# Kernel optimization log

Measured on AMD Instinct MI355X. Metric: run time of the kernel, lower is better.

## Reference

```python
import jax, jax.numpy as jnp
import numpy as np

N_NODES = 50000
N_EDGES = 800000
IN_CH = 128
OUT_CH = 64  # hidden = 2*OUT_CH = 128


def setup_inputs() -> dict:
    key = jax.random.key(0)
    ks = jax.random.split(key, 5)
    x = jax.random.normal(ks[0], (N_NODES, IN_CH), dtype=jnp.float32)
    edge_index = jax.random.randint(ks[1], (2, N_EDGES), 0, N_NODES, dtype=jnp.int32)
    # Glorot-ish scaled weights for the two GCNConv layers
    W1 = jax.random.normal(ks[2], (IN_CH, 2 * OUT_CH), dtype=jnp.float32) * 0.05
    b1 = jnp.zeros((2 * OUT_CH,), dtype=jnp.float32)
    W2 = jax.random.normal(ks[3], (2 * OUT_CH, OUT_CH), dtype=jnp.float32) * 0.05
    b2 = jnp.zeros((OUT_CH,), dtype=jnp.float32)
    return {"x": x, "edge_index": edge_index, "W1": W1, "b1": b1, "W2": W2, "b2": b2}


def reference(x, edge_index, W1, b1, W2, b2):
    N = x.shape[0]
    # GCN normalization with self-loops (PyG GCNConv default):
    # A_hat = A + I, deg from target nodes, norm = d_i^-1/2 * d_j^-1/2
    loops = jnp.arange(N, dtype=edge_index.dtype)
    row = jnp.concatenate([edge_index[0], loops])  # source
    col = jnp.concatenate([edge_index[1], loops])  # target
    deg = jax.ops.segment_sum(jnp.ones(row.shape, x.dtype), col, num_segments=N)
    dinv = jnp.where(deg > 0, jax.lax.rsqrt(deg), 0.0)
    norm = dinv[row] * dinv[col]  # [E+N]

    def conv(h, W, b):
        h = h @ W                           # [N, D_out] transform first (D_out <= D_in path)
        msg = norm[:, None] * h[row]        # gather + scale: [E+N, D_out]
        agg = jax.ops.segment_sum(msg, col, num_segments=N)
        return agg + b

    h = jax.nn.relu(conv(x, W1, b1))
    return conv(h, W2, b2)
```

## Files before the change

### kernel.cpp

```cpp
#include <hip/hip_runtime.h>
#include <hip/hip_bf16.h>
#include <hip/hip_fp16.h>

#define IN_CH  128
#define HID    128
#define OUTC   64

#define SCAN_CHUNK 2048
#define NBLK1 128
#define CHUNK2 6400
#define CAP2  6144

typedef _Float16 half8 __attribute__((ext_vector_type(8)));
typedef _Float16 half4v __attribute__((ext_vector_type(4)));
typedef float float4v __attribute__((ext_vector_type(4)));

__global__ __launch_bounds__(256) void histA_kernel(const int* __restrict__ dst,
                                                    int* __restrict__ hist,
                                                    int E, int NBK, int chunk) {
    __shared__ int h[256];
    int t = threadIdx.x;
    h[t] = 0;
    __syncthreads();
    int base = blockIdx.x * chunk;
    int end = base + chunk; if (end > E) end = E;
    for (int e = base + t; e < end; e += 256)
        atomicAdd(&h[dst[e] >> 8], 1);
    __syncthreads();
    if (t < NBK) hist[t * NBLK1 + blockIdx.x] = h[t];
}

__global__ __launch_bounds__(256) void gscanA_kernel(const int* __restrict__ arr,
                                                     int* __restrict__ bsum, int n) {
    __shared__ int red[256];
    int t = threadIdx.x;
    int base = blockIdx.x * SCAN_CHUNK + t * 8;
    int s = 0;
#pragma unroll
    for (int k = 0; k < 8; ++k) { int i = base + k; if (i < n) s += arr[i]; }
    red[t] = s;
    __syncthreads();
    for (int d = 128; d > 0; d >>= 1) {
        if (t < d) red[t] += red[t + d];
        __syncthreads();
    }
    if (t == 0) bsum[blockIdx.x] = red[0];
}

__global__ void gscanB_kernel(const int* __restrict__ bsum, int* __restrict__ boff, int nb) {
    if (threadIdx.x == 0 && blockIdx.x == 0) {
        int run = 0;
        for (int b = 0; b < nb; ++b) { boff[b] = run; run += bsum[b]; }
    }
}

__global__ __launch_bounds__(256) void gscanC_kernel(int* __restrict__ arr,
                                                     const int* __restrict__ boff, int n) {
    __shared__ int sums[256];
    int t = threadIdx.x;
    int base = blockIdx.x * SCAN_CHUNK + t * 8;
    int c[8];
    int s = 0;
#pragma unroll
    for (int k = 0; k < 8; ++k) { int i = base + k; c[k] = (i < n) ? arr[i] : 0; s += c[k]; }
    sums[t] = s;
    __syncthreads();
    for (int d = 1; d < 256; d <<= 1) {
        int v = (t >= d) ? sums[t - d] : 0;
        __syncthreads();
        sums[t] += v;
        __syncthreads();
    }
    int run = boff[blockIdx.x] + ((t == 0) ? 0 : sums[t - 1]);
#pragma unroll
    for (int k = 0; k < 8; ++k) {
        int i = base + k;
        if (i < n) { arr[i] = run; run += c[k]; }
    }
}

__global__ __launch_bounds__(256) void scatter2_kernel(const int* __restrict__ src,
                                                       const int* __restrict__ dst,
                                                       const int* __restrict__ HS,
                                                       unsigned* __restrict__ tmp,
                                                       int E, int NBK, int chunk) {
    __shared__ unsigned ein[CHUNK2];
    __shared__ unsigned eout[CHUNK2];
    __shared__ int h[256], lex[256], cur[256], hs[256];
    int t = threadIdx.x, blk = blockIdx.x;
    int base = blk * chunk;
    int end = base + chunk; if (end > E) end = E;
    int n = end - base;

    h[t] = 0;
    if (t < NBK) hs[t] = HS[t * NBLK1 + blk];
    __syncthreads();
    for (int i = t; i < n; i += 256) {
        unsigned d = (unsigned)dst[base + i];
        unsigned s = (unsigned)src[base + i];
        unsigned v = (d << 16) | s;
        ein[i] = v;
        atomicAdd(&h[d >> 8], 1);
    }
    __syncthreads();
    int c = h[t];
    for (int d = 1; d < 256; d <<= 1) {
        int v = (t >= d) ? h[t - d] : 0;
        __syncthreads();
        h[t] += v;
        __syncthreads();
    }
    lex[t] = h[t] - c;
    cur[t] = h[t] - c;
    __syncthreads();
    for (int i = t; i < n; i += 256) {
        unsigned v = ein[i];
        int pos = atomicAdd(&cur[v >> 24], 1);
        eout[pos] = v;
    }
    __syncthreads();
    for (int i = t; i < n; i += 256) {
        unsigned v = eout[i];
        int b = v >> 24;
        tmp[hs[b] + i - lex[b]] = v;
    }
}

__global__ __launch_bounds__(256) void csr2_kernel(const unsigned* __restrict__ tmp,
                                                   const int* __restrict__ HS,
                                                   int* __restrict__ off,
                                                   ushort* __restrict__ srcs,
                                                   float* __restrict__ dinv,
                                                   int E, int N, int NBK) {
    __shared__ int h[256];
    __shared__ int cur[256];
    __shared__ ushort outb[CAP2];
    int b = blockIdx.x, t = threadIdx.x;
    int lo = HS[b * NBLK1];
    int hi = (b + 1 < NBK) ? HS[(b + 1) * NBLK1] : E;

    h[t] = 0;
    __syncthreads();
    for (int i = lo + t; i < hi; i += 256)
        atomicAdd(&h[(tmp[i] >> 16) & 255], 1);
    __syncthreads();
    int c = h[t];
    for (int d = 1; d < 256; d <<= 1) {
        int v = (t >= d) ? h[t - d] : 0;
        __syncthreads();
        h[t] += v;
        __syncthreads();
    }
    int excl = h[t] - c;
    int node = (b << 8) + t;
    if (node < N) {
        off[node] = lo + excl;
        dinv[node] = rsqrtf((float)(c + 1));
    }
    if (b == NBK - 1 && t == 0) off[N] = E;
    cur[t] = excl;
    __syncthreads();
    for (int i = lo + t; i < hi; i += 256) {
        unsigned v = tmp[i];
        int pos = atomicAdd(&cur[(v >> 16) & 255], 1);
        if (pos < CAP2) outb[pos] = (ushort)(v & 0xFFFFu);
        else srcs[lo + pos] = (ushort)(v & 0xFFFFu);
    }
    __syncthreads();
    int cnt_b = hi - lo; if (cnt_b > CAP2) cnt_b = CAP2;
    for (int i = t; i < cnt_b; i += 256) srcs[lo + i] = outb[i];
}

__global__ void prep_kernel(const float* __restrict__ x,
                            const float* __restrict__ dinv,
                            _Float16* __restrict__ xhs,
                            const float* __restrict__ W1, const float* __restrict__ W2,
                            _Float16* __restrict__ Wt1, _Float16* __restrict__ Wt2,
                            int n4) {
    int i = blockIdx.x * 256 + threadIdx.x;
    if (i < n4) {
        float d = dinv[i >> 5];
        float4 v = ((const float4*)x)[i];
        half4v o = { (_Float16)(d * v.x), (_Float16)(d * v.y),
                     (_Float16)(d * v.z), (_Float16)(d * v.w) };
        ((half4v*)xhs)[i] = o;
    } else {
        int j = i - n4;
        if (j < 128 * 128) {
            int k = j >> 7, nn = j & 127;
            Wt1[nn * 128 + k] = (_Float16)W1[j];
        } else if (j < 128 * 128 + 128 * 64) {
            int jj = j - 128 * 128;
            int k = jj >> 6, nn = jj & 63;
            Wt2[nn * 128 + k] = (_Float16)W2[jj];
        }
    }
}

template <int NC, bool BIASRELU, bool SCALE>
__global__ __launch_bounds__(256) void mfma_gemm_kernel(const _Float16* A,
                                                        const _Float16* __restrict__ Wt,
                                                        const float* __restrict__ bias,
                                                        const float* __restrict__ dinv,
                                                        _Float16* Y, int N) {
    int wave = threadIdx.x >> 6;
    int lane = threadIdx.x & 63;
    int n16 = lane & 15;
    int q   = lane >> 4;
    int rowBase = blockIdx.x * 128 + wave * 32;

    half8 a[2][4];
#pragma unroll
    for (int rt = 0; rt < 2; ++rt) {
        int row = rowBase + rt * 16 + n16;
        if (row >= N) row = N - 1;
        const _Float16* ap = A + (size_t)row * 128 + q * 8;
#pragma unroll
        for (int kb = 0; kb < 4; ++kb)
            a[rt][kb] = *(const half8*)(ap + kb * 32);
    }

    constexpr int NT = NC / 16;
    float4v acc[2][NT];
#pragma unroll
    for (int rt = 0; rt < 2; ++rt)
#pragma unroll
        for (int ct = 0; ct < NT; ++ct) acc[rt][ct] = (float4v)0.f;

#pragma unroll
    for (int ct = 0; ct < NT; ++ct) {
        const _Float16* bp = Wt + (size_t)(ct * 16 + n16) * 128 + q * 8;
        half8 b[4];
#pragma unroll
        for (int kb = 0; kb < 4; ++kb) b[kb] = *(const half8*)(bp + kb * 32);
#pragma unroll
        for (int kb = 0; kb < 4; ++kb) {
            acc[0][ct] = __builtin_amdgcn_mfma_f32_16x16x32_f16(a[0][kb], b[kb], acc[0][ct], 0, 0, 0);
            acc[1][ct] = __builtin_amdgcn_mfma_f32_16x16x32_f16(a[1][kb], b[kb], acc[1][ct], 0, 0, 0);
        }
    }

#pragma unroll
    for (int rt = 0; rt < 2; ++rt) {
#pragma unroll
        for (int ct = 0; ct < NT; ++ct) {
            int col = ct * 16 + n16;
            float bv = BIASRELU ? bias[col] : 0.f;
#pragma unroll
            for (int r = 0; r < 4; ++r) {
                int row = rowBase + rt * 16 + q * 4 + r;
                if (row < N) {
                    float v = acc[rt][ct][r];
                    if (BIASRELU) v = fmaxf(v + bv, 0.f);
                    if (SCALE) v *= dinv[row];
                    Y[(size_t)row * NC + col] = (_Float16)v;
                }
            }
        }
    }
}

__global__ __launch_bounds__(256) void agg1_kernel(const _Float16* __restrict__ xhs,
                                                   const float* __restrict__ x,
                                                   const int* __restrict__ off,
                                                   const ushort* __restrict__ srcs,
                                                   const float* __restrict__ dinv,
                                                   _Float16* __restrict__ A1, int N) {
    int node = blockIdx.x * 4 + (threadIdx.x >> 6);
    if (node >= N) return;
    int lane = threadIdx.x & 63;
    int p = lane & 15;
    int g = lane >> 4;
    int s = off[node], e = off[node + 1];

    float acc[8];
#pragma unroll
    for (int i = 0; i < 8; ++i) acc[i] = 0.f;

    const half8* xs = (const half8*)xhs;
    int j = s;
    for (; j + 16 <= e; j += 16) {
        int i0 = srcs[j + g];
        int i1 = srcs[j + 4 + g];
        int i2 = srcs[j + 8 + g];
        int i3 = srcs[j + 12 + g];
        half8 u0 = xs[(size_t)i0 * 16 + p];
        half8 u1 = xs[(size_t)i1 * 16 + p];
        half8 u2 = xs[(size_t)i2 * 16 + p];
        half8 u3 = xs[(size_t)i3 * 16 + p];
#pragma unroll
        for (int i = 0; i < 8; ++i)
            acc[i] += ((float)u0[i] + (float)u1[i]) + ((float)u2[i] + (float)u3[i]);
    }
    for (; j < e; j += 4) {
        int jj = j + g;
        if (jj < e) {
            int i0 = srcs[jj];
            half8 u0 = xs[(size_t)i0 * 16 + p];
#pragma unroll
            for (int i = 0; i < 8; ++i) acc[i] += (float)u0[i];
        }
    }
#pragma unroll
    for (int i = 0; i < 8; ++i) {
        acc[i] += __shfl_xor(acc[i], 16, 64);
        acc[i] += __shfl_xor(acc[i], 32, 64);
    }
    if (g == 0) {
        float di = dinv[node];
        const float4* xr = (const float4*)(x + (size_t)node * 128);
        float4 s0 = xr[2 * p], s1 = xr[2 * p + 1];
        half8 h;
        h[0] = (_Float16)(di * (acc[0] + di * s0.x));
        h[1] = (_Float16)(di * (acc[1] + di * s0.y));
        h[2] = (_Float16)(di * (acc[2] + di * s0.z));
        h[3] = (_Float16)(di * (acc[3] + di * s0.w));
        h[4] = (_Float16)(di * (acc[4] + di * s1.x));
        h[5] = (_Float16)(di * (acc[5] + di * s1.y));
        h[6] = (_Float16)(di * (acc[6] + di * s1.z));
        h[7] = (_Float16)(di * (acc[7] + di * s1.w));
        *((half8*)(A1 + (size_t)node * 128) + p) = h;
    }
}

__global__ __launch_bounds__(256) void agg2_kernel(const _Float16* __restrict__ H3s,
                                                   const int* __restrict__ off,
                                                   const ushort* __restrict__ srcs,
                                                   const float* __restrict__ dinv,
                                                   const float* __restrict__ bias,
                                                   float* __restrict__ out, int N) {
    int node = blockIdx.x * 4 + (threadIdx.x >> 6);
    if (node >= N) return;
    int lane = threadIdx.x & 63;
    int p = lane & 7;
    int g = lane >> 3;
    int s = off[node], e = off[node + 1];

    float acc[8];
#pragma unroll
    for (int i = 0; i < 8; ++i) acc[i] = 0.f;

    const half8* hs = (const half8*)H3s;
    int j = s;
    for (; j + 16 <= e; j += 16) {
        int i0 = srcs[j + g];
        int i1 = srcs[j + 8 + g];
        half8 u0 = hs[(size_t)i0 * 8 + p];
        half8 u1 = hs[(size_t)i1 * 8 + p];
#pragma unroll
        for (int i = 0; i < 8; ++i) acc[i] += (float)u0[i] + (float)u1[i];
    }
    for (; j < e; j += 8) {
        int jj = j + g;
        if (jj < e) {
            int i0 = srcs[jj];
            half8 u0 = hs[(size_t)i0 * 8 + p];
#pragma unroll
            for (int i = 0; i < 8; ++i) acc[i] += (float)u0[i];
        }
    }
#pragma unroll
    for (int i = 0; i < 8; ++i) {
        acc[i] += __shfl_xor(acc[i], 8, 64);
        acc[i] += __shfl_xor(acc[i], 16, 64);
        acc[i] += __shfl_xor(acc[i], 32, 64);
    }
    if (g == 0) {
        float di = dinv[node];
        half8 sv = hs[(size_t)node * 8 + p];
        const float4* bp = (const float4*)(bias + p * 8);
        float4 b0 = bp[0], b1 = bp[1];
        float4 o0, o1;
        o0.x = di * (acc[0] + (float)sv[0]) + b0.x;
        o0.y = di * (acc[1] + (float)sv[1]) + b0.y;
        o0.z = di * (acc[2] + (float)sv[2]) + b0.z;
        o0.w = di * (acc[3] + (float)sv[3]) + b0.w;
        o1.x = di * (acc[4] + (float)sv[4]) + b1.x;
        o1.y = di * (acc[5] + (float)sv[5]) + b1.y;
        o1.z = di * (acc[6] + (float)sv[6]) + b1.z;
        o1.w = di * (acc[7] + (float)sv[7]) + b1.w;
        float4* op = (float4*)(out + (size_t)node * 64 + p * 8);
        op[0] = o0; op[1] = o1;
    }
}

extern "C" void kernel_launch(void* const* d_in, const int* in_sizes, int n_in,
                              void* d_out, int out_size, void* d_ws, size_t ws_size,
                              hipStream_t stream) {
    const float* x   = (const float*)d_in[0];
    const int*   ei  = (const int*)d_in[1];
    const float* W1  = (const float*)d_in[2];
    const float* b1  = (const float*)d_in[3];
    const float* W2  = (const float*)d_in[4];
    const float* b2  = (const float*)d_in[5];
    float* out = (float*)d_out;

    const int N = in_sizes[0] / IN_CH;
    const int E = in_sizes[1] / 2;
    const int* src = ei;
    const int* dst = ei + E;

    const int NBK = (N + 255) >> 8;
    const int M   = NBK * NBLK1;
    const int NB2 = (M + SCAN_CHUNK - 1) / SCAN_CHUNK;
    const int chunk = (E + NBLK1 - 1) / NBLK1;

    auto align256 = [](size_t v) { return (v + 255) & ~(size_t)255; };
    char* w = (char*)d_ws;
    int* off = (int*)w;              w += align256((size_t)(N + 1) * 4);
    ushort* srcs = (ushort*)w;       w += align256((size_t)E * 2);
    float* dinv = (float*)w;         w += align256((size_t)N * 4);
    int* hist = (int*)w;             w += align256((size_t)M * 4);
    int* bs2 = (int*)w;              w += align256((size_t)NB2 * 4);
    int* bo2 = (int*)w;              w += align256((size_t)NB2 * 4);
    _Float16* Wt1 = (_Float16*)w;    w += align256((size_t)HID * 128 * 2);
    _Float16* Wt2 = (_Float16*)w;    w += align256((size_t)OUTC * 128 * 2);
    _Float16* A1 = (_Float16*)w;
    unsigned* tmp = (unsigned*)w;
    w += align256((size_t)N * HID * 2);
    _Float16* xhs = (_Float16*)w;
    _Float16* H3s = (_Float16*)w;
    w += align256((size_t)N * HID * 2);

    histA_kernel<<<NBLK1, 256, 0, stream>>>(dst, hist, E, NBK, chunk);
    gscanA_kernel<<<NB2, 256, 0, stream>>>(hist, bs2, M);
    gscanB_kernel<<<1, 64, 0, stream>>>(bs2, bo2, NB2);
    gscanC_kernel<<<NB2, 256, 0, stream>>>(hist, bo2, M);
    scatter2_kernel<<<NBLK1, 256, 0, stream>>>(src, dst, hist, tmp, E, NBK, chunk);
    csr2_kernel<<<NBK, 256, 0, stream>>>(tmp, hist, off, srcs, dinv, E, N, NBK);

    int n4 = N * IN_CH / 4;
    int prep_grid = (n4 + 128 * 128 + 128 * 64 + 255) / 256;
    prep_kernel<<<prep_grid, 256, 0, stream>>>(x, dinv, xhs, W1, W2, Wt1, Wt2, n4);

    agg1_kernel<<<(N + 3) / 4, 256, 0, stream>>>(xhs, x, off, srcs, dinv, A1, N);
    mfma_gemm_kernel<HID, true, false><<<(N + 127) / 128, 256, 0, stream>>>(A1, Wt1, b1, nullptr, A1, N);

    mfma_gemm_kernel<OUTC, false, true><<<(N + 127) / 128, 256, 0, stream>>>(A1, Wt2, nullptr, dinv, H3s, N);
    agg2_kernel<<<(N + 3) / 4, 256, 0, stream>>>(H3s, off, srcs, dinv, b2, out, N);
}
```

Baseline: 212.7 us.

## Fuse CSR build into cooperative megakernel and fuse two GEMMs via LDS

Replaces the seven preprocessing launches (histogram, three-stage scan, scatter, CSR build, prep) with one cooperative kernel that uses grid.sync between phases. This removes launch gaps and tiny serial kernels. The two MFMA GEMMs are also fused: the ReLU'd hidden tile is staged in shared memory and multiplied by W2 directly, which avoids writing and re-reading A1. The costs are grid-wide barriers on only 256 blocks, a large static LDS footprint in the megakernel, and a strided elementwise prep loop.

```diff
diff --git a/kernel.cpp b/kernel.cpp
--- a/kernel.cpp
+++ b/kernel.cpp
@@ -1,101 +1,83 @@
 #include <hip/hip_runtime.h>
 #include <hip/hip_bf16.h>
 #include <hip/hip_fp16.h>
+#include <hip/hip_cooperative_groups.h>
+
+namespace cg = cooperative_groups;
 
 #define IN_CH  128
 #define HID    128
 #define OUTC   64
 
-#define SCAN_CHUNK 2048
-#define NBLK1 128
-#define CHUNK2 6400
-#define CAP2  6144
+#define GRIDC  256
+#define EMAX_CHUNK 3200
+#define CAP2   6144
 
 typedef _Float16 half8 __attribute__((ext_vector_type(8)));
 typedef _Float16 half4v __attribute__((ext_vector_type(4)));
 typedef float float4v __attribute__((ext_vector_type(4)));
 
-__global__ __launch_bounds__(256) void histA_kernel(const int* __restrict__ dst,
-                                                    int* __restrict__ hist,
-                                                    int E, int NBK, int chunk) {
-    __shared__ int h[256];
-    int t = threadIdx.x;
+__global__ __launch_bounds__(256) void mega_kernel(
+        const int* __restrict__ src, const int* __restrict__ dst,
+        int* __restrict__ hist, int* __restrict__ bsum, int* __restrict__ boff,
+        int* __restrict__ off, ushort* __restrict__ srcs, float* __restrict__ dinv,
+        unsigned* __restrict__ tmp,
+        const float* __restrict__ x, _Float16* __restrict__ xhs,
+        const float* __restrict__ W1, const float* __restrict__ W2,
+        _Float16* __restrict__ Wt1, _Float16* __restrict__ Wt2,
+        int E, int N, int NBK) {
+    cg::grid_group grid = cg::this_grid();
+    __shared__ int h[256], cur[256], lex[256], hs[256];
+    __shared__ unsigned ein[EMAX_CHUNK], eout[EMAX_CHUNK];
+    __shared__ ushort outb[CAP2];
+
+    int t = threadIdx.x, blk = blockIdx.x;
+    const int chunkE = (E + GRIDC - 1) / GRIDC;
+    int base = blk * chunkE;
+    int end = base + chunkE; if (end > E) end = E;
+
     h[t] = 0;
     __syncthreads();
-    int base = blockIdx.x * chunk;
-    int end = base + chunk; if (end > E) end = E;
     for (int e = base + t; e < end; e += 256)
         atomicAdd(&h[dst[e] >> 8], 1);
     __syncthreads();
-    if (t < NBK) hist[t * NBLK1 + blockIdx.x] = h[t];
-}
-
-__global__ __launch_bounds__(256) void gscanA_kernel(const int* __restrict__ arr,
-                                                     int* __restrict__ bsum, int n) {
-    __shared__ int red[256];
-    int t = threadIdx.x;
-    int base = blockIdx.x * SCAN_CHUNK + t * 8;
-    int s = 0;
-#pragma unroll
-    for (int k = 0; k < 8; ++k) { int i = base + k; if (i < n) s += arr[i]; }
-    red[t] = s;
-    __syncthreads();
-    for (int d = 128; d > 0; d >>= 1) {
-        if (t < d) red[t] += red[t + d];
-        __syncthreads();
-    }
-    if (t == 0) bsum[blockIdx.x] = red[0];
-}
-
-__global__ void gscanB_kernel(const int* __restrict__ bsum, int* __restrict__ boff, int nb) {
-    if (threadIdx.x == 0 && blockIdx.x == 0) {
-        int run = 0;
-        for (int b = 0; b < nb; ++b) { boff[b] = run; run += bsum[b]; }
-    }
-}
-
-__global__ __launch_bounds__(256) void gscanC_kernel(int* __restrict__ arr,
-                                                     const int* __restrict__ boff, int n) {
-    __shared__ int sums[256];
-    int t = threadIdx.x;
-    int base = blockIdx.x * SCAN_CHUNK + t * 8;
-    int c[8];
-    int s = 0;
-#pragma unroll
-    for (int k = 0; k < 8; ++k) { int i = base + k; c[k] = (i < n) ? arr[i] : 0; s += c[k]; }
-    sums[t] = s;
+    if (t < NBK) hist[t * GRIDC + blk] = h[t];
+    grid.sync();
+
+    int v2 = (t < NBK) ? hist[blk * NBK + t] : 0;
+    h[t] = v2;
     __syncthreads();
     for (int d = 1; d < 256; d <<= 1) {
-        int v = (t >= d) ? sums[t - d] : 0;
-        __syncthreads();
-        sums[t] += v;
-        __syncthreads();
-    }
-    int run = boff[blockIdx.x] + ((t == 0) ? 0 : sums[t - 1]);
-#pragma unroll
-    for (int k = 0; k < 8; ++k) {
-        int i = base + k;
-        if (i < n) { arr[i] = run; run += c[k]; }
-    }
-}
-
-__global__ __launch_bounds__(256) void scatter2_kernel(const int* __restrict__ src,
-                                                       const int* __restrict__ dst,
-                                                       const int* __restrict__ HS,
-                                                       unsigned* __restrict__ tmp,
-                                                       int E, int NBK, int chunk) {
-    __shared__ unsigned ein[CHUNK2];
-    __shared__ unsigned eout[CHUNK2];
-    __shared__ int h[256], lex[256], cur[256], hs[256];
-    int t = threadIdx.x, blk = blockIdx.x;
-    int base = blk * chunk;
-    int end = base + chunk; if (end > E) end = E;
-    int n = end - base;
+        int u = (t >= d) ? h[t - d] : 0;
+        __syncthreads();
+        h[t] += u;
+        __syncthreads();
+    }
+    if (t == 255) bsum[blk] = h[255];
+    grid.sync();
+
+    if (blk == 0) {
+        int bv = bsum[t];
+        cur[t] = bv;
+        __syncthreads();
+        for (int d = 1; d < 256; d <<= 1) {
+            int u = (t >= d) ? cur[t - d] : 0;
+            __syncthreads();
+            cur[t] += u;
+            __syncthreads();
+        }
+        boff[t] = cur[t] - bv;
+    }
+    grid.sync();
+
+    if (t < NBK) hist[blk * NBK + t] = boff[blk] + (h[t] - v2);
+    grid.sync();
 
     h[t] = 0;
-    if (t < NBK) hs[t] = HS[t * NBLK1 + blk];
-    __syncthreads();
-    for (int i = t; i < n; i += 256) {
+    if (t < NBK) hs[t] = hist[t * GRIDC + blk];
+    __syncthreads();
+    int n3 = end - base;
+    for (int i = t; i < n3; i += 256) {
         unsigned d = (unsigned)dst[base + i];
         unsigned s = (unsigned)src[base + i];
         unsigned v = (d << 16) | s;
@@ -103,158 +85,83 @@
         atomicAdd(&h[d >> 8], 1);
     }
     __syncthreads();
-    int c = h[t];
+    int c3 = h[t];
     for (int d = 1; d < 256; d <<= 1) {
-        int v = (t >= d) ? h[t - d] : 0;
-        __syncthreads();
-        h[t] += v;
-        __syncthreads();
-    }
-    lex[t] = h[t] - c;
-    cur[t] = h[t] - c;
-    __syncthreads();
-    for (int i = t; i < n; i += 256) {
+        int u = (t >= d) ? h[t - d] : 0;
+        __syncthreads();
+        h[t] += u;
+        __syncthreads();
+    }
+    lex[t] = h[t] - c3;
+    cur[t] = h[t] - c3;
+    __syncthreads();
+    for (int i = t; i < n3; i += 256) {
         unsigned v = ein[i];
         int pos = atomicAdd(&cur[v >> 24], 1);
         eout[pos] = v;
     }
     __syncthreads();
-    for (int i = t; i < n; i += 256) {
+    for (int i = t; i < n3; i += 256) {
         unsigned v = eout[i];
         int b = v >> 24;
         tmp[hs[b] + i - lex[b]] = v;
     }
-}
-
-__global__ __launch_bounds__(256) void csr2_kernel(const unsigned* __restrict__ tmp,
-                                                   const int* __restrict__ HS,
-                                                   int* __restrict__ off,
-                                                   ushort* __restrict__ srcs,
-                                                   float* __restrict__ dinv,
-                                                   int E, int N, int NBK) {
-    __shared__ int h[256];
-    __shared__ int cur[256];
-    __shared__ ushort outb[CAP2];
-    int b = blockIdx.x, t = threadIdx.x;
-    int lo = HS[b * NBLK1];
-    int hi = (b + 1 < NBK) ? HS[(b + 1) * NBLK1] : E;
-
-    h[t] = 0;
-    __syncthreads();
-    for (int i = lo + t; i < hi; i += 256)
-        atomicAdd(&h[(tmp[i] >> 16) & 255], 1);
-    __syncthreads();
-    int c = h[t];
-    for (int d = 1; d < 256; d <<= 1) {
-        int v = (t >= d) ? h[t - d] : 0;
-        __syncthreads();
-        h[t] += v;
-        __syncthreads();
-    }
-    int excl = h[t] - c;
-    int node = (b << 8) + t;
-    if (node < N) {
-        off[node] = lo + excl;
-        dinv[node] = rsqrtf((float)(c + 1));
-    }
-    if (b == NBK - 1 && t == 0) off[N] = E;
-    cur[t] = excl;
-    __syncthreads();
-    for (int i = lo + t; i < hi; i += 256) {
-        unsigned v = tmp[i];
-        int pos = atomicAdd(&cur[(v >> 16) & 255], 1);
-        if (pos < CAP2) outb[pos] = (ushort)(v & 0xFFFFu);
-        else srcs[lo + pos] = (ushort)(v & 0xFFFFu);
-    }
-    __syncthreads();
-    int cnt_b = hi - lo; if (cnt_b > CAP2) cnt_b = CAP2;
-    for (int i = t; i < cnt_b; i += 256) srcs[lo + i] = outb[i];
-}
-
-__global__ void prep_kernel(const float* __restrict__ x,
-                            const float* __restrict__ dinv,
-                            _Float16* __restrict__ xhs,
-                            const float* __restrict__ W1, const float* __restrict__ W2,
-                            _Float16* __restrict__ Wt1, _Float16* __restrict__ Wt2,
-                            int n4) {
-    int i = blockIdx.x * 256 + threadIdx.x;
-    if (i < n4) {
-        float d = dinv[i >> 5];
-        float4 v = ((const float4*)x)[i];
-        half4v o = { (_Float16)(d * v.x), (_Float16)(d * v.y),
-                     (_Float16)(d * v.z), (_Float16)(d * v.w) };
-        ((half4v*)xhs)[i] = o;
-    } else {
-        int j = i - n4;
-        if (j < 128 * 128) {
-            int k = j >> 7, nn = j & 127;
-            Wt1[nn * 128 + k] = (_Float16)W1[j];
-        } else if (j < 128 * 128 + 128 * 64) {
-            int jj = j - 128 * 128;
-            int k = jj >> 6, nn = jj & 63;
-            Wt2[nn * 128 + k] = (_Float16)W2[jj];
-        }
-    }
-}
-
-template <int NC, bool BIASRELU, bool SCALE>
-__global__ __launch_bounds__(256) void mfma_gemm_kernel(const _Float16* A,
-                                                        const _Float16* __restrict__ Wt,
-                                                        const float* __restrict__ bias,
-                                                        const float* __restrict__ dinv,
-                                                        _Float16* Y, int N) {
-    int wave = threadIdx.x >> 6;
-    int lane = threadIdx.x & 63;
-    int n16 = lane & 15;
-    int q   = lane >> 4;
-    int rowBase = blockIdx.x * 128 + wave * 32;
-
-    half8 a[2][4];
-#pragma unroll
-    for (int rt = 0; rt < 2; ++rt) {
-        int row = rowBase + rt * 16 + n16;
-        if (row >= N) row = N - 1;
-        const _Float16* ap = A + (size_t)row * 128 + q * 8;
-#pragma unroll
-        for (int kb = 0; kb < 4; ++kb)
-            a[rt][kb] = *(const half8*)(ap + kb * 32);
-    }
-
-    constexpr int NT = NC / 16;
-    float4v acc[2][NT];
-#pragma unroll
-    for (int rt = 0; rt < 2; ++rt)
-#pragma unroll
-        for (int ct = 0; ct < NT; ++ct) acc[rt][ct] = (float4v)0.f;
-
-#pragma unroll
-    for (int ct = 0; ct < NT; ++ct) {
-        const _Float16* bp = Wt + (size_t)(ct * 16 + n16) * 128 + q * 8;
-        half8 b[4];
-#pragma unroll
-        for (int kb = 0; kb < 4; ++kb) b[kb] = *(const half8*)(bp + kb * 32);
-#pragma unroll
-        for (int kb = 0; kb < 4; ++kb) {
-            acc[0][ct] = __builtin_amdgcn_mfma_f32_16x16x32_f16(a[0][kb], b[kb], acc[0][ct], 0, 0, 0);
-            acc[1][ct] = __builtin_amdgcn_mfma_f32_16x16x32_f16(a[1][kb], b[kb], acc[1][ct], 0, 0, 0);
-        }
-    }
-
-#pragma unroll
-    for (int rt = 0; rt < 2; ++rt) {
-#pragma unroll
-        for (int ct = 0; ct < NT; ++ct) {
-            int col = ct * 16 + n16;
-            float bv = BIASRELU ? bias[col] : 0.f;
-#pragma unroll
-            for (int r = 0; r < 4; ++r) {
-                int row = rowBase + rt * 16 + q * 4 + r;
-                if (row < N) {
-                    float v = acc[rt][ct][r];
-                    if (BIASRELU) v = fmaxf(v + bv, 0.f);
-                    if (SCALE) v *= dinv[row];
-                    Y[(size_t)row * NC + col] = (_Float16)v;
-                }
+    grid.sync();
+
+    if (blk < NBK) {
+        int lo = hist[blk * GRIDC];
+        int hi = (blk + 1 < NBK) ? hist[(blk + 1) * GRIDC] : E;
+        h[t] = 0;
+        __syncthreads();
+        for (int i = lo + t; i < hi; i += 256)
+            atomicAdd(&h[(tmp[i] >> 16) & 255], 1);
+        __syncthreads();
+        int c = h[t];
+        for (int d = 1; d < 256; d <<= 1) {
+            int u = (t >= d) ? h[t - d] : 0;
+            __syncthreads();
+            h[t] += u;
+            __syncthreads();
+        }
+        int excl = h[t] - c;
+        int node = (blk << 8) + t;
+        if (node < N) {
+            off[node] = lo + excl;
+            dinv[node] = rsqrtf((float)(c + 1));
+        }
+        if (blk == NBK - 1 && t == 0) off[N] = E;
+        cur[t] = excl;
+        __syncthreads();
+        for (int i = lo + t; i < hi; i += 256) {
+            unsigned v = tmp[i];
+            int pos = atomicAdd(&cur[(v >> 16) & 255], 1);
+            if (pos < CAP2) outb[pos] = (ushort)(v & 0xFFFFu);
+            else srcs[lo + pos] = (ushort)(v & 0xFFFFu);
+        }
+        __syncthreads();
+        int cnt_b = hi - lo; if (cnt_b > CAP2) cnt_b = CAP2;
+        for (int i = t; i < cnt_b; i += 256) srcs[lo + i] = outb[i];
+    }
+    grid.sync();
+
+    int n4 = N * (IN_CH / 4);
+    int total = n4 + 128 * 128 + 128 * 64;
+    for (int i = blk * 256 + t; i < total; i += GRIDC * 256) {
+        if (i < n4) {
+            float d = dinv[i >> 5];
+            float4 v = ((const float4*)x)[i];
+            half4v o = { (_Float16)(d * v.x), (_Float16)(d * v.y),
+                         (_Float16)(d * v.z), (_Float16)(d * v.w) };
+            ((half4v*)xhs)[i] = o;
+        } else {
+            int j = i - n4;
+            if (j < 128 * 128) {
+                int k = j >> 7, nn = j & 127;
+                Wt1[nn * 128 + k] = (_Float16)W1[j];
+            } else {
+                int jj = j - 128 * 128;
+                int k = jj >> 6, nn = jj & 63;
+                Wt2[nn * 128 + k] = (_Float16)W2[jj];
             }
         }
     }
@@ -310,17 +217,114 @@
         float di = dinv[node];
         const float4* xr = (const float4*)(x + (size_t)node * 128);
         float4 s0 = xr[2 * p], s1 = xr[2 * p + 1];
-        half8 h;
-        h[0] = (_Float16)(di * (acc[0] + di * s0.x));
-        h[1] = (_Float16)(di * (acc[1] + di * s0.y));
-        h[2] = (_Float16)(di * (acc[2] + di * s0.z));
-        h[3] = (_Float16)(di * (acc[3] + di * s0.w));
-        h[4] = (_Float16)(di * (acc[4] + di * s1.x));
-        h[5] = (_Float16)(di * (acc[5] + di * s1.y));
-        h[6] = (_Float16)(di * (acc[6] + di * s1.z));
-        h[7] = (_Float16)(di * (acc[7] + di * s1.w));
-        *((half8*)(A1 + (size_t)node * 128) + p) = h;
-    }
+        half8 hh;
+        hh[0] = (_Float16)(di * (acc[0] + di * s0.x));
+        hh[1] = (_Float16)(di * (acc[1] + di * s0.y));
+        hh[2] = (_Float16)(di * (acc[2] + di * s0.z));
+        hh[3] = (_Float16)(di * (acc[3] + di * s0.w));
+        hh[4] = (_Float16)(di * (acc[4] + di * s1.x));
+        hh[5] = (_Float16)(di * (acc[5] + di * s1.y));
+        hh[6] = (_Float16)(di * (acc[6] + di * s1.z));
+        hh[7] = (_Float16)(di * (acc[7] + di * s1.w));
+        *((half8*)(A1 + (size_t)node * 128) + p) = hh;
+    }
+}
+
+#define TSTRIDE 140
+__global__ __launch_bounds__(256) void gemm_fused_kernel(
+        const _Float16* __restrict__ A1, const _Float16* __restrict__ Wt1,
+        const float* __restrict__ b1, const _Float16* __restrict__ Wt2,
+        const float* __restrict__ dinv, _Float16* __restrict__ H3s, int N) {
+    __shared__ _Float16 tile[4][32 * TSTRIDE];
+    int wave = threadIdx.x >> 6;
+    int lane = threadIdx.x & 63;
+    int n16 = lane & 15;
+    int q   = lane >> 4;
+    int rowBase = blockIdx.x * 128 + wave * 32;
+
+    half8 a[2][4];
+#pragma unroll
+    for (int rt = 0; rt < 2; ++rt) {
+        int row = rowBase + rt * 16 + n16;
+        if (row >= N) row = N - 1;
+        const _Float16* ap = A1 + (size_t)row * 128 + q * 8;
+#pragma unroll
+        for (int kb = 0; kb < 4; ++kb)
+            a[rt][kb] = *(const half8*)(ap + kb * 32);
+    }
+
+    float4v acc1[2][8];
+#pragma unroll
+    for (int rt = 0; rt < 2; ++rt)
+#pragma unroll
+        for (int ct = 0; ct < 8; ++ct) acc1[rt][ct] = (float4v)0.f;
+#pragma unroll
+    for (int ct = 0; ct < 8; ++ct) {
+        const _Float16* bp = Wt1 + (size_t)(ct * 16 + n16) * 128 + q * 8;
+        half8 b[4];
+#pragma unroll
+        for (int kb = 0; kb < 4; ++kb) b[kb] = *(const half8*)(bp + kb * 32);
+#pragma unroll
+        for (int kb = 0; kb < 4; ++kb) {
+            acc1[0][ct] = __builtin_amdgcn_mfma_f32_16x16x32_f16(a[0][kb], b[kb], acc1[0][ct], 0, 0, 0);
+            acc1[1][ct] = __builtin_amdgcn_mfma_f32_16x16x32_f16(a[1][kb], b[kb], acc1[1][ct], 0, 0, 0);
+        }
+    }
+
+    _Float16* tw = &tile[wave][0];
+#pragma unroll
+    for (int ct = 0; ct < 8; ++ct) {
+        int col = ct * 16 + n16;
+        float bv = b1[col];
+#pragma unroll
+        for (int rt = 0; rt < 2; ++rt)
+#pragma unroll
+            for (int r = 0; r < 4; ++r) {
+                int row = rt * 16 + q * 4 + r;
+                tw[row * TSTRIDE + col] = (_Float16)fmaxf(acc1[rt][ct][r] + bv, 0.f);
+            }
+    }
+    __syncthreads();
+
+    half8 a2[2][4];
+#pragma unroll
+    for (int rt = 0; rt < 2; ++rt) {
+        const _Float16* tp = tw + (rt * 16 + n16) * TSTRIDE + q * 8;
+#pragma unroll
+        for (int kb = 0; kb < 4; ++kb)
+            a2[rt][kb] = *(const half8*)(tp + kb * 32);
+    }
+
+    float4v acc2[2][4];
+#pragma unroll
+    for (int rt = 0; rt < 2; ++rt)
+#pragma unroll
+        for (int ct = 0; ct < 4; ++ct) acc2[rt][ct] = (float4v)0.f;
+#pragma unroll
+    for (int ct = 0; ct < 4; ++ct) {
+        const _Float16* bp = Wt2 + (size_t)(ct * 16 + n16) * 128 + q * 8;
+        half8 b[4];
+#pragma unroll
+        for (int kb = 0; kb < 4; ++kb) b[kb] = *(const half8*)(bp + kb * 32);
+#pragma unroll
+        for (int kb = 0; kb < 4; ++kb) {
+            acc2[0][ct] = __builtin_amdgcn_mfma_f32_16x16x32_f16(a2[0][kb], b[kb], acc2[0][ct], 0, 0, 0);
+            acc2[1][ct] = __builtin_amdgcn_mfma_f32_16x16x32_f16(a2[1][kb], b[kb], acc2[1][ct], 0, 0, 0);
+        }
+    }
+
+#pragma unroll
+    for (int rt = 0; rt < 2; ++rt)
+#pragma unroll
+        for (int ct = 0; ct < 4; ++ct) {
+            int col = ct * 16 + n16;
+#pragma unroll
+            for (int r = 0; r < 4; ++r) {
+                int row = rowBase + rt * 16 + q * 4 + r;
+                if (row < N)
+                    H3s[(size_t)row * OUTC + col] = (_Float16)(acc2[rt][ct][r] * dinv[row]);
+            }
+        }
 }
 
 __global__ __launch_bounds__(256) void agg2_kernel(const _Float16* __restrict__ H3s,
@@ -395,15 +399,13 @@
     const float* b2  = (const float*)d_in[5];
     float* out = (float*)d_out;
 
-    const int N = in_sizes[0] / IN_CH;
-    const int E = in_sizes[1] / 2;
+    int N = in_sizes[0] / IN_CH;
+    int E = in_sizes[1] / 2;
     const int* src = ei;
     const int* dst = ei + E;
 
-    const int NBK = (N + 255) >> 8;
-    const int M   = NBK * NBLK1;
-    const int NB2 = (M + SCAN_CHUNK - 1) / SCAN_CHUNK;
-    const int chunk = (E + NBLK1 - 1) / NBLK1;
+    int NBK = (N + 255) >> 8;
+    const int M = NBK * GRIDC;
 
     auto align256 = [](size_t v) { return (v + 255) & ~(size_t)255; };
     char* w = (char*)d_ws;
@@ -411,8 +413,8 @@
     ushort* srcs = (ushort*)w;       w += align256((size_t)E * 2);
     float* dinv = (float*)w;         w += align256((size_t)N * 4);
     int* hist = (int*)w;             w += align256((size_t)M * 4);
-    int* bs2 = (int*)w;              w += align256((size_t)NB2 * 4);
-    int* bo2 = (int*)w;              w += align256((size_t)NB2 * 4);
+    int* bsum = (int*)w;             w += align256((size_t)GRIDC * 4);
+    int* boff = (int*)w;             w += align256((size_t)GRIDC * 4);
     _Float16* Wt1 = (_Float16*)w;    w += align256((size_t)HID * 128 * 2);
     _Float16* Wt2 = (_Float16*)w;    w += align256((size_t)OUTC * 128 * 2);
     _Float16* A1 = (_Float16*)w;
@@ -422,20 +424,16 @@
     _Float16* H3s = (_Float16*)w;
     w += align256((size_t)N * HID * 2);
 
-    histA_kernel<<<NBLK1, 256, 0, stream>>>(dst, hist, E, NBK, chunk);
-    gscanA_kernel<<<NB2, 256, 0, stream>>>(hist, bs2, M);
-    gscanB_kernel<<<1, 64, 0, stream>>>(bs2, bo2, NB2);
-    gscanC_kernel<<<NB2, 256, 0, stream>>>(hist, bo2, M);
-    scatter2_kernel<<<NBLK1, 256, 0, stream>>>(src, dst, hist, tmp, E, NBK, chunk);
-    csr2_kernel<<<NBK, 256, 0, stream>>>(tmp, hist, off, srcs, dinv, E, N, NBK);
-
-    int n4 = N * IN_CH / 4;
-    int prep_grid = (n4 + 128 * 128 + 128 * 64 + 255) / 256;
-    prep_kernel<<<prep_grid, 256, 0, stream>>>(x, dinv, xhs, W1, W2, Wt1, Wt2, n4);
+    void* args[] = {
+        (void*)&src, (void*)&dst, (void*)&hist, (void*)&bsum, (void*)&boff,
+        (void*)&off, (void*)&srcs, (void*)&dinv, (void*)&tmp,
+        (void*)&x, (void*)&xhs, (void*)&W1, (void*)&W2,
+        (void*)&Wt1, (void*)&Wt2, (void*)&E, (void*)&N, (void*)&NBK
+    };
+    hipLaunchCooperativeKernel((const void*)mega_kernel, dim3(GRIDC), dim3(256),
+                               args, 0, stream);
 
     agg1_kernel<<<(N + 3) / 4, 256, 0, stream>>>(xhs, x, off, srcs, dinv, A1, N);
-    mfma_gemm_kernel<HID, true, false><<<(N + 127) / 128, 256, 0, stream>>>(A1, Wt1, b1, nullptr, A1, N);
-
-    mfma_gemm_kernel<OUTC, false, true><<<(N + 127) / 128, 256, 0, stream>>>(A1, Wt2, nullptr, dinv, H3s, N);
+    gemm_fused_kernel<<<(N + 127) / 128, 256, 0, stream>>>(A1, Wt1, b1, Wt2, dinv, H3s, N);
     agg2_kernel<<<(N + 3) / 4, 256, 0, stream>>>(H3s, off, srcs, dinv, b2, out, N);
 }
```

Result: slower. 383.3 us (+80.2%).
